# Kernel optimization log

Hardware: AMD Instinct MI355X
Metric: run time of the kernel (lower is better)

The kernel has to match this reference:

```python
import jax, jax.numpy as jnp
import numpy as np


def setup_inputs() -> dict:
    key = jax.random.key(0)
    k1, k2, k3, k4 = jax.random.split(key, 4)
    pi = np.float32(np.pi)
    return {
        "bii": pi * jax.random.uniform(k1, (1,), dtype=jnp.float32),
        "bjj": pi * jax.random.uniform(k2, (1,), dtype=jnp.float32),
        "bij_real": pi * jax.random.uniform(k3, (1,), dtype=jnp.float32),
        "bij_img": pi * jax.random.uniform(k4, (1,), dtype=jnp.float32),
        "conn_i": 123,
        "conn_j": 4567,
        "N": 8192,
    }


def _block_exp(bii, bjj, bij_real, bij_img):
    """Closed-form exp(1j*H) for Hermitian 2x2 H = [[a, c],[conj(c), b]].

    exp(1j*H) = e^{1j*t} * (cos(r) I + 1j * sin(r)/r * (H - t I)),
    t = (a+b)/2, r = sqrt(((a-b)/2)^2 + |c|^2). Exact since B is zero
    outside the 2x2 block, matching torch.matrix_exp(1j*B).
    """
    a = bii[0]
    b = bjj[0]
    cr = bij_real[0]
    ci = bij_img[0]
    t = 0.5 * (a + b)
    d = 0.5 * (a - b)
    r = jnp.sqrt(d * d + cr * cr + ci * ci)
    safe_r = jnp.where(r > 0, r, jnp.ones_like(r))
    sinc = jnp.where(r > 0, jnp.sin(r) / safe_r, jnp.ones_like(r))
    cosr = jnp.cos(r)
    phase = jnp.exp(1j * t.astype(jnp.complex64))  # complex64 scalar
    c = (cr + 1j * ci).astype(jnp.complex64)
    e_ii = phase * (cosr + 1j * sinc * d)
    e_jj = phase * (cosr - 1j * sinc * d)
    e_ij = phase * (1j * sinc) * c
    e_ji = phase * (1j * sinc) * jnp.conj(c)
    return e_ii, e_jj, e_ij, e_ji


def reference(bii, bjj, bij_real, bij_img, conn_i, conn_j, N):
    e_ii, e_jj, e_ij, e_ji = _block_exp(bii, bjj, bij_real, bij_img)
    V = jnp.eye(N, dtype=jnp.complex64)
    rows = jnp.array([conn_i, conn_j, conn_i, conn_j])
    cols = jnp.array([conn_i, conn_j, conn_j, conn_i])
    vals = jnp.stack([e_ii, e_jj, e_ij, e_ji]).astype(jnp.complex64)
    V = V.at[rows, cols].set(vals)
    return V
```

## Files before the change

### kernel.cpp

```cpp
#include <hip/hip_runtime.h>
#include <math.h>

typedef float vfloat4 __attribute__((ext_vector_type(4)));

__global__ void fill_identity_kernel(vfloat4* __restrict__ out, int out_size,
                                     const int* __restrict__ Np) {
    const int n = Np[0];
    const int stride = out_size / n;
    const int mult = stride / n;
    const int ls = 31 - __clz(stride);

    const size_t f = ((size_t)blockIdx.x * blockDim.x + threadIdx.x) * 4;
    if (f >= (size_t)out_size) return;

    const int row = (int)(f >> ls);
    const int o = (int)(f & (size_t)(stride - 1));

    vfloat4 v = {0.f, 0.f, 0.f, 0.f};
    const int k = row * mult - o;
    if (k >= 0 && k < 4) v[k] = 1.0f;

    __builtin_nontemporal_store(v, out + (f >> 2));
}

__global__ void patch_block_kernel(float* __restrict__ out, int out_size,
                                   const float* __restrict__ bii,
                                   const float* __restrict__ bjj,
                                   const float* __restrict__ bij_real,
                                   const float* __restrict__ bij_img,
                                   const int* __restrict__ conn_i,
                                   const int* __restrict__ conn_j,
                                   const int* __restrict__ Np) {
    if (threadIdx.x != 0 || blockIdx.x != 0) return;

    const int n = Np[0];
    const int stride = out_size / n;
    const int mult = stride / n;

    const float a  = bii[0];
    const float b  = bjj[0];
    const float cr = bij_real[0];
    const float ci = bij_img[0];

    const float t = 0.5f * (a + b);
    const float d = 0.5f * (a - b);
    const float r = sqrtf(d * d + cr * cr + ci * ci);
    const float sinc = (r > 0.f) ? (sinf(r) / r) : 1.0f;
    const float cosr = cosf(r);
    const float pr = cosf(t);
    const float pi = sinf(t);

    const float sd = sinc * d;
    const float eii_r = pr * cosr - pi * sd;
    const float eii_i = pr * sd + pi * cosr;
    const float ejj_r = pr * cosr + pi * sd;
    const float ejj_i = -pr * sd + pi * cosr;
    const float sc_r = -sinc * ci;
    const float sc_i = sinc * cr;
    const float eij_r = pr * sc_r - pi * sc_i;
    const float eij_i = pr * sc_i + pi * sc_r;
    const float sj_r = sinc * ci;
    const float sj_i = sinc * cr;
    const float eji_r = pr * sj_r - pi * sj_i;
    const float eji_i = pr * sj_i + pi * sj_r;

    const int i = conn_i[0];
    const int j = conn_j[0];

    if (mult == 2) {
        size_t idx;
        idx = (size_t)i * stride + 2 * (size_t)i; out[idx] = eii_r; out[idx + 1] = eii_i;
        idx = (size_t)j * stride + 2 * (size_t)j; out[idx] = ejj_r; out[idx + 1] = ejj_i;
        idx = (size_t)i * stride + 2 * (size_t)j; out[idx] = eij_r; out[idx + 1] = eij_i;
        idx = (size_t)j * stride + 2 * (size_t)i; out[idx] = eji_r; out[idx + 1] = eji_i;
    } else {
        out[(size_t)i * stride + i] = eii_r;
        out[(size_t)j * stride + j] = ejj_r;
        out[(size_t)i * stride + j] = eij_r;
        out[(size_t)j * stride + i] = eji_r;
    }
}

extern "C" void kernel_launch(void* const* d_in, const int* in_sizes, int n_in,
                              void* d_out, int out_size, void* d_ws, size_t ws_size,
                              hipStream_t stream) {
    const float* bii      = (const float*)d_in[0];
    const float* bjj      = (const float*)d_in[1];
    const float* bij_real = (const float*)d_in[2];
    const float* bij_img  = (const float*)d_in[3];
    const int*   conn_i   = (const int*)d_in[4];
    const int*   conn_j   = (const int*)d_in[5];
    const int*   Np       = (const int*)d_in[6];

    float* out = (float*)d_out;

    const int n_f4 = out_size >> 2;
    const int blocks = (n_f4 + 255) / 256;
    fill_identity_kernel<<<dim3(blocks), dim3(256), 0, stream>>>(
        (vfloat4*)out, out_size, Np);

    patch_block_kernel<<<dim3(1), dim3(64), 0, stream>>>(
        out, out_size, bii, bjj, bij_real, bij_img, conn_i, conn_j, Np);
}
```

Before: 270.0 us.

## Zero output with memset and fuse diagonal writes with block patch kernel

Replaces the custom vectorized identity-fill kernel with hipMemsetAsync to zero the matrix. A single small kernel then writes the diagonal ones, skipping rows i and j, and thread 0 patches the 2x2 block. This leans on the runtime's memset path for the 512 MB zero fill and merges two launches into one. The cost is extra scattered diagonal writes after the memset and reliance on how fast the runtime memset is compared with the nontemporal stores.

```diff
diff --git a/kernel.cpp b/kernel.cpp
--- a/kernel.cpp
+++ b/kernel.cpp
@@ -1,41 +1,33 @@
 #include <hip/hip_runtime.h>
 #include <math.h>
 
-typedef float vfloat4 __attribute__((ext_vector_type(4)));
-
-__global__ void fill_identity_kernel(vfloat4* __restrict__ out, int out_size,
-                                     const int* __restrict__ Np) {
+__global__ __launch_bounds__(256) void diag_patch_kernel(
+    float* __restrict__ out, int out_size,
+    const float* __restrict__ bii,
+    const float* __restrict__ bjj,
+    const float* __restrict__ bij_real,
+    const float* __restrict__ bij_img,
+    const int* __restrict__ conn_i,
+    const int* __restrict__ conn_j,
+    const int* __restrict__ Np)
+{
     const int n = Np[0];
     const int stride = out_size / n;
     const int mult = stride / n;
-    const int ls = 31 - __clz(stride);
 
-    const size_t f = ((size_t)blockIdx.x * blockDim.x + threadIdx.x) * 4;
-    if (f >= (size_t)out_size) return;
+    const int i = conn_i[0];
+    const int j = conn_j[0];
 
-    const int row = (int)(f >> ls);
-    const int o = (int)(f & (size_t)(stride - 1));
+    const int gid = blockIdx.x * blockDim.x + threadIdx.x;
+    const int nth = gridDim.x * blockDim.x;
 
-    vfloat4 v = {0.f, 0.f, 0.f, 0.f};
-    const int k = row * mult - o;
-    if (k >= 0 && k < 4) v[k] = 1.0f;
+    for (int r = gid; r < n; r += nth) {
+        if (r != i && r != j) {
+            out[(size_t)r * stride + (size_t)mult * r] = 1.0f;
+        }
+    }
 
-    __builtin_nontemporal_store(v, out + (f >> 2));
-}
-
-__global__ void patch_block_kernel(float* __restrict__ out, int out_size,
-                                   const float* __restrict__ bii,
-                                   const float* __restrict__ bjj,
-                                   const float* __restrict__ bij_real,
-                                   const float* __restrict__ bij_img,
-                                   const int* __restrict__ conn_i,
-                                   const int* __restrict__ conn_j,
-                                   const int* __restrict__ Np) {
-    if (threadIdx.x != 0 || blockIdx.x != 0) return;
-
-    const int n = Np[0];
-    const int stride = out_size / n;
-    const int mult = stride / n;
+    if (gid != 0) return;
 
     const float a  = bii[0];
     const float b  = bjj[0];
@@ -64,9 +56,6 @@
     const float eji_r = pr * sj_r - pi * sj_i;
     const float eji_i = pr * sj_i + pi * sj_r;
 
-    const int i = conn_i[0];
-    const int j = conn_j[0];
-
     if (mult == 2) {
         size_t idx;
         idx = (size_t)i * stride + 2 * (size_t)i; out[idx] = eii_r; out[idx + 1] = eii_i;
@@ -94,11 +83,8 @@
 
     float* out = (float*)d_out;
 
-    const int n_f4 = out_size >> 2;
-    const int blocks = (n_f4 + 255) / 256;
-    fill_identity_kernel<<<dim3(blocks), dim3(256), 0, stream>>>(
-        (vfloat4*)out, out_size, Np);
+    hipMemsetAsync(d_out, 0, (size_t)out_size * sizeof(float), stream);
 
-    patch_block_kernel<<<dim3(1), dim3(64), 0, stream>>>(
+    diag_patch_kernel<<<dim3(64), dim3(256), 0, stream>>>(
         out, out_size, bii, bjj, bij_real, bij_img, conn_i, conn_j, Np);
 }
```

New measurement: 261.9 us. -3.0%, faster.
